# Kernel optimization log

Measured on AMD Instinct MI355X. Metric: run time of the kernel, lower is better.

The kernel has to match this reference:

```python
import jax, jax.numpy as jnp
import numpy as np

DIM = 1024
HEADS = 16
HEAD_DIM = DIM // HEADS
HIDDEN = int(DIM * 4.0)
EPS = 1e-5


def setup_inputs() -> dict:
    key = jax.random.key(0)
    ks = jax.random.split(key, 16)
    s = 0.02
    inp = {
        'x': jax.random.normal(ks[0], (2, 2048, DIM), dtype=jnp.float32),
        'g1': jnp.ones((DIM,), jnp.float32),
        'b1': jnp.zeros((DIM,), jnp.float32),
        'Wq': jax.random.normal(ks[1], (DIM, DIM)) * s,
        'bq': jnp.zeros((DIM,), jnp.float32),
        'Wk': jax.random.normal(ks[2], (DIM, DIM)) * s,
        'bk': jnp.zeros((DIM,), jnp.float32),
        'Wv': jax.random.normal(ks[3], (DIM, DIM)) * s,
        'bv': jnp.zeros((DIM,), jnp.float32),
        'Wo': jax.random.normal(ks[4], (DIM, DIM)) * s,
        'bo': jnp.zeros((DIM,), jnp.float32),
        'g2': jnp.ones((DIM,), jnp.float32),
        'b2': jnp.zeros((DIM,), jnp.float32),
        'W1': jax.random.normal(ks[5], (DIM, HIDDEN)) * s,
        'bf1': jnp.zeros((HIDDEN,), jnp.float32),
        'W2': jax.random.normal(ks[6], (HIDDEN, DIM)) * s,
        'bf2': jnp.zeros((DIM,), jnp.float32),
    }
    return inp


def _layernorm(x, g, b):
    mu = jnp.mean(x, axis=-1, keepdims=True)
    var = jnp.mean((x - mu) ** 2, axis=-1, keepdims=True)
    return (x - mu) * jax.lax.rsqrt(var + EPS) * g + b


def _block(x, g1, b1, Wq, bq, Wk, bk, Wv, bv, Wo, bo, g2, b2, W1, bf1, W2, bf2):
    B, N, C = x.shape
    h = _layernorm(x, g1, b1)
    # project and split heads: [B, H, N, D]
    q = (h @ Wq + bq).reshape(B, N, HEADS, HEAD_DIM).transpose(0, 2, 1, 3)
    k = (h @ Wk + bk).reshape(B, N, HEADS, HEAD_DIM).transpose(0, 2, 1, 3)
    v = (h @ Wv + bv).reshape(B, N, HEADS, HEAD_DIM).transpose(0, 2, 1, 3)
    scale = HEAD_DIM ** -0.5
    attn = jnp.einsum('bhqd,bhkd->bhqk', q, k) * scale
    attn = jax.nn.softmax(attn, axis=-1)
    o = jnp.einsum('bhqk,bhkd->bhqd', attn, v)
    o = o.transpose(0, 2, 1, 3).reshape(B, N, C)
    x = x + (o @ Wo + bo)
    h = _layernorm(x, g2, b2)
    h = jax.nn.gelu(h @ W1 + bf1, approximate=False)
    x = x + (h @ W2 + bf2)
    return x


def reference(x, g1, b1, Wq, bq, Wk, bk, Wv, bv, Wo, bo, g2, b2, W1, bf1, W2, bf2):
    return _block(x, g1, b1, Wq, bq, Wk, bk, Wv, bv, Wo, bo, g2, b2, W1, bf1, W2, bf2)
```

## Files before the change

### kernel.cpp

```cpp
#include <hip/hip_runtime.h>
#include <hip/hip_bf16.h>
#include <math.h>


typedef unsigned short ushort_t;
typedef short short8 __attribute__((ext_vector_type(8)));
typedef float f32x4 __attribute__((ext_vector_type(4)));

#define TOKENS 4096
#define SEQ    2048
#define DIMC   1024
#define HID    4096

__device__ __forceinline__ float bf2f(ushort_t u) {
    union { float f; unsigned int u; } c; c.u = ((unsigned int)u) << 16; return c.f;
}
__device__ __forceinline__ ushort_t f2bf(float f) {
    union { float f; unsigned int u; } c; c.f = f;
    unsigned int u = c.u;
    unsigned int r = u + 0x7fffu + ((u >> 16) & 1u);
    return (ushort_t)(r >> 16);
}
__device__ __forceinline__ float gelu_f(float x) {
    const float y = 0.79788456080286536f * (x + 0.044715f * x * x * x);
    const float t = __expf(-2.0f * fabsf(y));
    const float th = (1.0f - t) / (1.0f + t);
    return 0.5f * x * (1.0f + copysignf(th, y));
}
__device__ __forceinline__ float load_elem(const void* p, size_t i, int isbf) {
    return isbf ? bf2f(((const ushort_t*)p)[i]) : ((const float*)p)[i];
}

__global__ __launch_bounds__(256) void detect_dtype(
    const ushort_t* __restrict__ x, int* __restrict__ flag)
{
    __shared__ int bad;
    if (threadIdx.x == 0) bad = 0;
    __syncthreads();
    for (int i = threadIdx.x; i < 4096; i += 256) {
        float v = bf2f(x[i]);
        if (!(fabsf(v) <= 1e6f)) bad = 1;
    }
    __syncthreads();
    if (threadIdx.x == 0) { flag[0] = (bad == 0) ? 1 : 0; flag[1] = 1; }
}

__global__ __launch_bounds__(256) void transpose_w_all(
    const void* __restrict__ Wq, const void* __restrict__ Wk,
    const void* __restrict__ Wv, const void* __restrict__ Wo,
    const void* __restrict__ W1, const void* __restrict__ W2,
    ushort_t* __restrict__ wsq, ushort_t* __restrict__ w1t,
    ushort_t* __restrict__ w2t, const int* __restrict__ flag)
{
    __shared__ ushort_t tile[32][33];
    const int isbf = *flag;
    const int id = blockIdx.x;
    const void* in; ushort_t* out; int K, N, bx, by;
    if (id < 4096) {
        const int z = id >> 10, t = id & 1023;
        in = z == 0 ? Wq : (z == 1 ? Wk : (z == 2 ? Wv : Wo));
        out = wsq + (size_t)z * DIMC * DIMC;
        K = DIMC; N = DIMC; bx = t & 31; by = t >> 5;
    } else if (id < 8192) {
        const int t = id - 4096;
        in = W1; out = w1t; K = DIMC; N = HID;
        bx = t & 127; by = t >> 7;
    } else {
        const int t = id - 8192;
        in = W2; out = w2t; K = HID; N = DIMC;
        bx = t & 31; by = t >> 5;
    }
    const int kb = by * 32, nb = bx * 32;
    const int tx = threadIdx.x & 31, ty = threadIdx.x >> 5;
    for (int i = 0; i < 4; i++) {
        int k = kb + ty + i * 8;
        tile[ty + i * 8][tx] = f2bf(load_elem(in, (size_t)k * N + nb + tx, isbf));
    }
    __syncthreads();
    for (int i = 0; i < 4; i++) {
        int n = nb + ty + i * 8;
        out[(size_t)n * K + kb + tx] = tile[tx][ty + i * 8];
    }
}

template<int INMODE>
__global__ __launch_bounds__(256) void ln_kernel(
    const void* __restrict__ in, const void* __restrict__ g,
    const void* __restrict__ b, const int* __restrict__ flag,
    ushort_t* __restrict__ out)
{
    const int isbf = *flag;
    const int t = blockIdx.x;
    const int tid = threadIdx.x;
    const size_t base = (size_t)t * DIMC;
    float v[4];
    for (int i = 0; i < 4; i++) {
        int idx = tid + i * 256;
        v[i] = (INMODE == 1) ? ((const float*)in)[base + idx]
                             : load_elem(in, base + idx, isbf);
    }
    float s  = v[0] + v[1] + v[2] + v[3];
    float s2 = v[0]*v[0] + v[1]*v[1] + v[2]*v[2] + v[3]*v[3];
    for (int off = 1; off < 64; off <<= 1) {
        s  += __shfl_xor(s,  off);
        s2 += __shfl_xor(s2, off);
    }
    __shared__ float red[8];
    const int wave = tid >> 6, lane = tid & 63;
    if (lane == 0) { red[wave] = s; red[wave + 4] = s2; }
    __syncthreads();
    s  = red[0] + red[1] + red[2] + red[3];
    s2 = red[4] + red[5] + red[6] + red[7];
    const float mu  = s * (1.0f / DIMC);
    const float var = s2 * (1.0f / DIMC) - mu * mu;
    const float inv = rsqrtf(fmaxf(var, 0.f) + 1e-5f);
    for (int i = 0; i < 4; i++) {
        int idx = tid + i * 256;
        float o = (v[i] - mu) * inv * load_elem(g, idx, isbf) + load_elem(b, idx, isbf);
        out[base + idx] = f2bf(o);
    }
}

__global__ __launch_bounds__(256) void reduce_ln(
    const float* __restrict__ p0, const float* __restrict__ p1,
    const void* __restrict__ bias, const void* __restrict__ resid,
    float* __restrict__ x1f, const void* __restrict__ g,
    const void* __restrict__ b, const int* __restrict__ flag,
    ushort_t* __restrict__ out)
{
    const int isbf = *flag;
    const int t = blockIdx.x;
    const int tid = threadIdx.x;
    const size_t base = (size_t)t * DIMC;
    const int col = tid * 4;
    const size_t i = base + col;
    const float4 a  = *(const float4*)&p0[i];
    const float4 bb = *(const float4*)&p1[i];
    float v[4] = {a.x + bb.x, a.y + bb.y, a.z + bb.z, a.w + bb.w};
    for (int c = 0; c < 4; c++) {
        v[c] += load_elem(bias, col + c, isbf);
        v[c] += load_elem(resid, i + c, isbf);
    }
    *(float4*)&x1f[i] = make_float4(v[0], v[1], v[2], v[3]);

    float s  = v[0] + v[1] + v[2] + v[3];
    float s2 = v[0]*v[0] + v[1]*v[1] + v[2]*v[2] + v[3]*v[3];
    for (int off = 1; off < 64; off <<= 1) {
        s  += __shfl_xor(s,  off);
        s2 += __shfl_xor(s2, off);
    }
    __shared__ float red[8];
    const int wave = tid >> 6, lane = tid & 63;
    if (lane == 0) { red[wave] = s; red[wave + 4] = s2; }
    __syncthreads();
    s  = red[0] + red[1] + red[2] + red[3];
    s2 = red[4] + red[5] + red[6] + red[7];
    const float mu  = s * (1.0f / DIMC);
    const float var = s2 * (1.0f / DIMC) - mu * mu;
    const float inv = rsqrtf(fmaxf(var, 0.f) + 1e-5f);
    ushort_t ob[4];
    for (int c = 0; c < 4; c++) {
        float o = (v[c] - mu) * inv * load_elem(g, col + c, isbf)
                + load_elem(b, col + c, isbf);
        ob[c] = f2bf(o);
    }
    unsigned int lo = (unsigned int)ob[0] | ((unsigned int)ob[1] << 16);
    unsigned int hi = (unsigned int)ob[2] | ((unsigned int)ob[3] << 16);
    *(uint2*)&out[i] = make_uint2(lo, hi);
}

template<int BN, int RES, int ACT, int OUTF, int NBUF>
__global__ __launch_bounds__(256) void gemm_bt(
    const ushort_t* __restrict__ A, const ushort_t* __restrict__ BT,
    const void* __restrict__ bias0, const void* __restrict__ bias1,
    const void* __restrict__ bias2, const void* __restrict__ resid,
    void* __restrict__ out0, void* __restrict__ out1, void* __restrict__ out2,
    int M, int N, int K, int Ksub, const int* __restrict__ flag)
{
    constexpr int BM   = 128;
    constexpr int JF   = BN / 32;
    constexpr int ASEG = BM / 16;
    constexpr int SPW  = (BM + BN) / 64;
    __shared__ __align__(16) ushort_t As[NBUF][BM][32];
    __shared__ __align__(16) ushort_t Bs[NBUF][BN][32];
    const int isbf = *flag;
    const int tid = threadIdx.x, lane = tid & 63, wave = tid >> 6;

    int bx, by;
    {
        const int gx = gridDim.x, gy = gridDim.y;
        const int nwg = gx * gy;
        const int orig = blockIdx.y * gx + blockIdx.x;
        const int cpx = nwg >> 3;
        const int swz = (orig & 7) * cpx + (orig >> 3);
        bx = swz % gx;
        by = swz / gx;
    }
    const int m0 = by * BM, n0 = bx * BN;
    const int wm = (wave & 1) * 64;
    const int wn = (wave >> 1) * (BN / 2);
    const int lm = lane & 15, quad = lane >> 4;

    const void* biasp = bias0;
    void* outp = out0;
    int nout = N;
    int colmask = 0x7fffffff;
    int sel = 0;
    if (OUTF == 3) {
        sel = n0 >> 10;
        biasp = sel == 0 ? bias0 : (sel == 1 ? bias1 : bias2);
        outp  = sel == 0 ? out0  : (sel == 1 ? out1  : out2);
        nout = 1024; colmask = 1023;
    }
    int kbeg = 0;
    if (OUTF == 4) {
        kbeg = blockIdx.z * Ksub;
        outp = blockIdx.z ? out1 : out0;
    }

    f32x4 acc[4][JF];
    for (int i = 0; i < 4; i++)
        for (int j = 0; j < JF; j++)
            acc[i][j] = (f32x4){0.f, 0.f, 0.f, 0.f};

    const int lsw  = lane ^ ((lane >> 3) & 7);
    const int lrow = lsw >> 2;
    const int lcol = (lsw & 3) * 8;
    const int srd  = (4 * lm + quad);
    const int srz  = srd ^ ((srd >> 3) & 7);
    const int rsw  = srz >> 2;
    const int csw  = (srz & 3) * 8;

    const ushort_t* gpp[SPW];
    ushort_t* lpp[NBUF][SPW];
#pragma unroll
    for (int s = 0; s < SPW; s++) {
        const int seg = wave * SPW + s;
        if (seg < ASEG) {
            gpp[s] = &A[(size_t)(m0 + seg * 16 + lrow) * K + kbeg + lcol];
#pragma unroll
            for (int bfi = 0; bfi < NBUF; bfi++) lpp[bfi][s] = &As[bfi][seg * 16][0];
        } else {
            gpp[s] = &BT[(size_t)(n0 + (seg - ASEG) * 16 + lrow) * K + kbeg + lcol];
#pragma unroll
            for (int bfi = 0; bfi < NBUF; bfi++) lpp[bfi][s] = &Bs[bfi][(seg - ASEG) * 16][0];
        }
    }

#define GEMM_STAGE(BUF, T)                                                    \
    {                                                                         \
        _Pragma("unroll")                                                     \
        for (int s = 0; s < SPW; s++)                                         \
            __builtin_amdgcn_global_load_lds(                                 \
                (const __attribute__((address_space(1))) unsigned int*)       \
                    (gpp[s] + (size_t)(T) * 32),                              \
                (__attribute__((address_space(3))) unsigned int*)lpp[BUF][s], \
                16, 0, 0);                                                    \
    }

#define GEMM_COMPUTE(BUF)                                                     \
    {                                                                         \
        short8 af[4], bfr[JF];                                                \
        _Pragma("unroll")                                                     \
        for (int i = 0; i < 4; i++)                                           \
            af[i] = *(const short8*)&As[BUF][wm + i * 16 + rsw][csw];         \
        _Pragma("unroll")                                                     \
        for (int j = 0; j < JF; j++)                                          \
            bfr[j] = *(const short8*)&Bs[BUF][wn + j * 16 + rsw][csw];        \
        _Pragma("unroll")                                                     \
        for (int i = 0; i < 4; i++)                                           \
            _Pragma("unroll")                                                 \
            for (int j = 0; j < JF; j++)                                      \
                acc[i][j] = __builtin_amdgcn_mfma_f32_16x16x32_bf16(          \
                    af[i], bfr[j], acc[i][j], 0, 0, 0);                       \
    }

#define GEMM_STEP(BC, BS, T)                                                  \
    if ((T) < nt) {                                                           \
        if ((T) + 1 < nt) {                                                   \
            if constexpr (SPW == 3)                                           \
                asm volatile("s_waitcnt vmcnt(3) lgkmcnt(0)" ::: "memory");   \
            else                                                              \
                asm volatile("s_waitcnt vmcnt(4) lgkmcnt(0)" ::: "memory");   \
        } else {                                                              \
            asm volatile("s_waitcnt vmcnt(0) lgkmcnt(0)" ::: "memory");       \
        }                                                                     \
        __builtin_amdgcn_s_barrier();                                         \
        __builtin_amdgcn_sched_barrier(0);                                    \
        if ((T) + 2 < nt) GEMM_STAGE(BS, (T) + 2);                            \
        __builtin_amdgcn_s_setprio(1);                                        \
        GEMM_COMPUTE(BC);                                                     \
        __builtin_amdgcn_s_setprio(0);                                        \
    }

    const int nt = Ksub / 32;
    if constexpr (NBUF == 3) {
        GEMM_STAGE(0, 0);
        GEMM_STAGE(1, 1);
        for (int t = 0; t < nt; t += 3) {
            GEMM_STEP(0, 2, t);
            GEMM_STEP(1, 0, t + 1);
            GEMM_STEP(2, 1, t + 2);
        }
    } else {
        GEMM_STAGE(0, 0);
        __syncthreads();
        for (int t = 0; t < nt; t += 2) {
            GEMM_STAGE(1, t + 1);
            GEMM_COMPUTE(0);
            __syncthreads();
            if (t + 2 < nt) GEMM_STAGE(0, t + 2);
            GEMM_COMPUTE(1);
            __syncthreads();
        }
    }
#undef GEMM_STEP
#undef GEMM_STAGE
#undef GEMM_COMPUTE

    if (OUTF == 3 && sel == 2) {
        for (int j = 0; j < JF; j++) {
            const int colo = (n0 + wn + j * 16 + lm) & 1023;
            const float bv = load_elem(biasp, colo, isbf);
            for (int i = 0; i < 4; i++) {
                const int token = m0 + wm + i * 16 + quad * 4;
                const int bb = token >> 11, ss = token & 2047;
                unsigned int lo = (unsigned int)f2bf(acc[i][j][0] + bv)
                                | ((unsigned int)f2bf(acc[i][j][1] + bv) << 16);
                unsigned int hi = (unsigned int)f2bf(acc[i][j][2] + bv)
                                | ((unsigned int)f2bf(acc[i][j][3] + bv) << 16);
                *(uint2*)&((ushort_t*)outp)[(size_t)((bb << 10) + colo) * SEQ + ss] =
                    make_uint2(lo, hi);
            }
        }
        return;
    }

    for (int j = 0; j < JF; j++) {
        const int col  = n0 + wn + j * 16 + lm;
        const int colo = col & colmask;
        const float bv = (OUTF == 4) ? 0.f : load_elem(biasp, colo, isbf);
        for (int i = 0; i < 4; i++) {
            const int rbase = m0 + wm + i * 16 + quad * 4;
            for (int r = 0; r < 4; r++) {
                const size_t oi = (size_t)(rbase + r) * nout + colo;
                float v2 = acc[i][j][r] + bv;
                if (ACT == 1) v2 = gelu_f(v2);
                if (RES == 1) v2 += load_elem(resid, oi, isbf);
                if (RES == 2) v2 += ((const float*)resid)[oi];
                if (OUTF == 1 || OUTF == 4) { ((float*)outp)[oi] = v2; }
                else if (OUTF == 2) {
                    if (isbf) ((ushort_t*)outp)[oi] = f2bf(v2);
                    else      ((float*)outp)[oi] = v2;
                }
                else                { ((ushort_t*)outp)[oi] = f2bf(v2); }
            }
        }
    }
}

template<int RESRAW, int OUTF32>
__global__ __launch_bounds__(256) void splitk_reduce(
    const float* __restrict__ p0, const float* __restrict__ p1,
    const void* __restrict__ bias, const void* __restrict__ resid,
    void* __restrict__ out, const int* __restrict__ flag)
{
    const int isbf = *flag;
    const size_t i = ((size_t)blockIdx.x * 256 + threadIdx.x) * 4;
    const float4 a = *(const float4*)&p0[i];
    const float4 b = *(const float4*)&p1[i];
    const int col = (int)(i & 1023);
    float v[4] = {a.x + b.x, a.y + b.y, a.z + b.z, a.w + b.w};
    for (int c = 0; c < 4; c++) {
        v[c] += load_elem(bias, col + c, isbf);
        v[c] += RESRAW ? load_elem(resid, i + c, isbf) : ((const float*)resid)[i + c];
    }
    if (OUTF32) {
        *(float4*)&((float*)out)[i] = make_float4(v[0], v[1], v[2], v[3]);
    } else if (isbf) {
        unsigned int lo = (unsigned int)f2bf(v[0]) | ((unsigned int)f2bf(v[1]) << 16);
        unsigned int hi = (unsigned int)f2bf(v[2]) | ((unsigned int)f2bf(v[3]) << 16);
        *(uint2*)&((ushort_t*)out)[i] = make_uint2(lo, hi);
    } else {
        *(float4*)&((float*)out)[i] = make_float4(v[0], v[1], v[2], v[3]);
    }
}

__global__ __launch_bounds__(256) void attn_kernel(
    const ushort_t* __restrict__ q, const ushort_t* __restrict__ k,
    const ushort_t* __restrict__ vt, ushort_t* __restrict__ o)
{
    const int bh = blockIdx.x;
    const int b  = bh >> 4, h = bh & 15;
    const int q0 = blockIdx.y * 128;
    const int tid = threadIdx.x, lane = tid & 63, wave = tid >> 6;
    const int lm = lane & 15, quad = lane >> 4;

    __shared__ ushort_t Qs[128][72];
    __shared__ ushort_t Ks[64][72];
    __shared__ ushort_t Vt[64][72];
    typedef ushort_t PsRow[32][72];
    PsRow* Ps = reinterpret_cast<PsRow*>(&Qs[0][0]);

    const size_t base  = ((size_t)b * SEQ) * DIMC + h * 64;
    const size_t vbase = ((size_t)b * DIMC + h * 64) * SEQ;

    {
        const int er0 = (tid * 8) >> 6;
        const int ec0 = (tid * 8) & 63;
        for (int half = 0; half < 4; half++) {
            const int r = er0 + half * 32;
            short8 qq = *(const short8*)&q[base + (size_t)(q0 + r) * DIMC + ec0];
            short8 qs;
            for (int i = 0; i < 8; i++)
                qs[i] = (short)f2bf(bf2f((ushort_t)qq[i]) * 0.18033688011112042f);
            *(short8*)&Qs[r][ec0] = qs;
        }
    }
    __syncthreads();

    short8 qf[2][2];
    for (int qh = 0; qh < 2; qh++)
        for (int ks = 0; ks < 2; ks++)
            qf[qh][ks] = *(const short8*)&Qs[wave * 32 + qh * 16 + lm][quad * 8 + ks * 32];

    short8 onef;
    for (int i = 0; i < 8; i++) onef[i] = (short)0x3F80;

    f32x4 oacc[4][2], lacc[2];
    for (int j = 0; j < 4; j++)
        for (int qh = 0; qh < 2; qh++) oacc[j][qh] = (f32x4){0.f, 0.f, 0.f, 0.f};
    lacc[0] = (f32x4){0.f, 0.f, 0.f, 0.f};
    lacc[1] = (f32x4){0.f, 0.f, 0.f, 0.f};

    const int er = (tid * 8) >> 6;
    const int ec = (tid * 8) & 63;
    const int dd = tid >> 2;
    const int kg = tid & 3;

    short8 kreg0, kreg1, vreg0, vreg1;
    {
        kreg0 = *(const short8*)&k[base + (size_t)(er) * DIMC + ec];
        kreg1 = *(const short8*)&k[base + (size_t)(er + 32) * DIMC + ec];
        const size_t vsrc = vbase + (size_t)dd * SEQ + kg * 16;
        vreg0 = *(const short8*)&vt[vsrc];
        vreg1 = *(const short8*)&vt[vsrc + 8];
    }

    for (int kt = 0; kt < SEQ / 64; kt++) {
        __syncthreads();
        *(short8*)&Ks[er][ec]          = kreg0;
        *(short8*)&Ks[er + 32][ec]     = kreg1;
        *(short8*)&Vt[dd][kg * 16]     = vreg0;
        *(short8*)&Vt[dd][kg * 16 + 8] = vreg1;
        __syncthreads();
        if (kt + 1 < SEQ / 64) {
            const int kn = (kt + 1) * 64;
            kreg0 = *(const short8*)&k[base + (size_t)(kn + er) * DIMC + ec];
            kreg1 = *(const short8*)&k[base + (size_t)(kn + er + 32) * DIMC + ec];
            const size_t vsrc = vbase + (size_t)dd * SEQ + kn + kg * 16;
            vreg0 = *(const short8*)&vt[vsrc];
            vreg1 = *(const short8*)&vt[vsrc + 8];
        }

        f32x4 st[4][2];
        for (int j = 0; j < 4; j++)
            for (int qh = 0; qh < 2; qh++) st[j][qh] = (f32x4){0.f, 0.f, 0.f, 0.f};
        for (int ks = 0; ks < 2; ks++) {
            for (int j = 0; j < 4; j++) {
                short8 kf = *(const short8*)&Ks[j * 16 + lm][quad * 8 + ks * 32];
                for (int qh = 0; qh < 2; qh++)
                    st[j][qh] = __builtin_amdgcn_mfma_f32_16x16x32_bf16(kf, qf[qh][ks], st[j][qh], 0, 0, 0);
            }
        }

        for (int j = 0; j < 4; j++)
            for (int qh = 0; qh < 2; qh++) {
                unsigned int u0 = __float_as_uint(__builtin_amdgcn_exp2f(st[j][qh][0]));
                unsigned int u1 = __float_as_uint(__builtin_amdgcn_exp2f(st[j][qh][1]));
                unsigned int u2 = __float_as_uint(__builtin_amdgcn_exp2f(st[j][qh][2]));
                unsigned int u3 = __float_as_uint(__builtin_amdgcn_exp2f(st[j][qh][3]));
                unsigned int lo = (u1 & 0xffff0000u) | (u0 >> 16);
                unsigned int hi = (u3 & 0xffff0000u) | (u2 >> 16);
                *(uint2*)&Ps[wave][qh * 16 + lm][j * 16 + quad * 4] = make_uint2(lo, hi);
            }

        for (int ks = 0; ks < 2; ks++) {
            for (int qh = 0; qh < 2; qh++) {
                short8 pf = *(const short8*)&Ps[wave][qh * 16 + lm][quad * 8 + ks * 32];
                lacc[qh] = __builtin_amdgcn_mfma_f32_16x16x32_bf16(pf, onef, lacc[qh], 0, 0, 0);
                for (int j = 0; j < 4; j++) {
                    short8 vf = *(const short8*)&Vt[j * 16 + lm][quad * 8 + ks * 32];
                    oacc[j][qh] = __builtin_amdgcn_mfma_f32_16x16x32_bf16(pf, vf, oacc[j][qh], 0, 0, 0);
                }
            }
        }
    }

    float rinv[2][4];
    for (int qh = 0; qh < 2; qh++)
        for (int r = 0; r < 4; r++) rinv[qh][r] = 1.0f / fmaxf(lacc[qh][r], 1e-30f);

    for (int j = 0; j < 4; j++)
        for (int qh = 0; qh < 2; qh++)
            for (int r = 0; r < 4; r++) {
                const int row = q0 + wave * 32 + qh * 16 + quad * 4 + r;
                o[base + (size_t)row * DIMC + j * 16 + lm] = f2bf(oacc[j][qh][r] * rinv[qh][r]);
            }
}

extern "C" void kernel_launch(void* const* d_in, const int* in_sizes, int n_in,
                              void* d_out, int out_size, void* d_ws, size_t ws_size,
                              hipStream_t stream)
{
    const void* x   = d_in[0];
    const void* g1  = d_in[1];
    const void* b1  = d_in[2];
    const void* Wq  = d_in[3];
    const void* bq  = d_in[4];
    const void* Wk  = d_in[5];
    const void* bk  = d_in[6];
    const void* Wv  = d_in[7];
    const void* bv  = d_in[8];
    const void* Wo  = d_in[9];
    const void* bo  = d_in[10];
    const void* g2  = d_in[11];
    const void* b2  = d_in[12];
    const void* W1  = d_in[13];
    const void* bf1 = d_in[14];
    const void* W2  = d_in[15];
    const void* bf2 = d_in[16];

    const size_t SZ_TOKD_BF = (size_t)TOKENS * DIMC * 2;
    const size_t SZ_TOKD_F  = (size_t)TOKENS * DIMC * 4;
    const size_t SZ_W_SQ    = (size_t)DIMC * DIMC * 2;
    const size_t SZ_W_FF    = (size_t)DIMC * HID * 2;
    const size_t SZ_FF1     = (size_t)TOKENS * HID * 2;

    char* ws = (char*)d_ws;
    size_t off = 0;
    int*      flag = (int*)(ws + off);       off += 256;
    ushort_t* h    = (ushort_t*)(ws + off);  off += SZ_TOKD_BF;
    ushort_t* qb   = (ushort_t*)(ws + off);  off += SZ_TOKD_BF;
    ushort_t* kb_  = (ushort_t*)(ws + off);  off += SZ_TOKD_BF;
    ushort_t* ao   = (ushort_t*)(ws + off);  off += SZ_TOKD_BF;
    ushort_t* vtg  = (ushort_t*)(ws + off);  off += SZ_TOKD_BF;
    float*    x1f  = (float*)qb;
    float*    pa   = (float*)qb;
    float*    p0   = (float*)ao;
    ushort_t* wqt  = (ushort_t*)(ws + off);  off += SZ_W_SQ;
    ushort_t* wkt  = (ushort_t*)(ws + off);  off += SZ_W_SQ;
    ushort_t* wvt  = (ushort_t*)(ws + off);  off += SZ_W_SQ;
    ushort_t* wot  = (ushort_t*)(ws + off);  off += SZ_W_SQ;
    ushort_t* w1t  = (ushort_t*)(ws + off);  off += SZ_W_FF;
    ushort_t* w2t  = (ushort_t*)(ws + off);  off += SZ_W_FF;
    ushort_t* ff1  = (ushort_t*)(ws + off);  off += SZ_FF1;
    float*    p1   = (float*)(ws + off);     off += SZ_TOKD_F;
    if (ws_size < off) return;

    (void)wkt; (void)wvt;

    detect_dtype<<<1, 256, 0, stream>>>((const ushort_t*)x, flag);

    transpose_w_all<<<12288, 256, 0, stream>>>(Wq, Wk, Wv, Wo, W1, W2,
                                               wqt, w1t, w2t, flag);

    ln_kernel<0><<<TOKENS, 256, 0, stream>>>(x, g1, b1, flag, h);

    gemm_bt<128, 0, 0, 3, 3><<<dim3(24, 32), 256, 0, stream>>>(
        h, wqt, bq, bk, bv, nullptr, qb, kb_, vtg, TOKENS, 3072, DIMC, DIMC, flag);

    attn_kernel<<<dim3(32, 16), 256, 0, stream>>>(qb, kb_, vtg, ao);

    gemm_bt<64, 0, 0, 4, 3><<<dim3(16, 32, 2), 256, 0, stream>>>(
        ao, wot, nullptr, nullptr, nullptr, nullptr, pa, p1, nullptr,
        TOKENS, DIMC, DIMC, DIMC / 2, flag);

    reduce_ln<<<TOKENS, 256, 0, stream>>>(
        pa, p1, bo, x, x1f, g2, b2, flag, h);

    gemm_bt<128, 0, 1, 0, 3><<<dim3(32, 32), 256, 0, stream>>>(
        h, w1t, bf1, nullptr, nullptr, nullptr, ff1, nullptr, nullptr,
        TOKENS, HID, DIMC, DIMC, flag);

    gemm_bt<64, 0, 0, 4, 3><<<dim3(16, 32, 2), 256, 0, stream>>>(
        ff1, w2t, nullptr, nullptr, nullptr, nullptr, p0, p1, nullptr,
        TOKENS, DIMC, HID, HID / 2, flag);

    splitk_reduce<0, 0><<<TOKENS * DIMC / 1024, 256, 0, stream>>>(
        p0, p1, bf2, x1f, d_out, flag);
}
```

Measured before the change: 397.6 us.

## Halve attention query tile to 64 rows and swizzle block order

The attention kernel now handles 64 query rows per block (16 per wave) instead of 128, doubling the grid to 1024 blocks. A block-index swizzle groups adjacent blocks onto the same head to improve K/V cache reuse. The aim is more parallelism and occupancy across the CUs, at the cost of loading each K/V tile twice as often per query. The split-K GEMM also gains support for up to four z-slices, but no launch uses more than two.

Result: slower. 415.7 us (+4.6%).

```diff
diff --git a/kernel.cpp b/kernel.cpp
--- a/kernel.cpp
+++ b/kernel.cpp
@@ -214,8 +214,9 @@
     }
     int kbeg = 0;
     if (OUTF == 4) {
-        kbeg = blockIdx.z * Ksub;
-        outp = blockIdx.z ? out1 : out0;
+        const int z = blockIdx.z;
+        kbeg = z * Ksub;
+        outp = z == 0 ? out0 : (z == 1 ? out1 : (z == 2 ? out2 : (void*)resid));
     }
 
     f32x4 acc[4][JF];
@@ -390,16 +391,22 @@
     const ushort_t* __restrict__ q, const ushort_t* __restrict__ k,
     const ushort_t* __restrict__ vt, ushort_t* __restrict__ o)
 {
-    const int bh = blockIdx.x;
+    int qtile, bh;
+    {
+        const int orig = blockIdx.y * 32 + blockIdx.x;
+        const int swz = (orig & 7) * 128 + (orig >> 3);
+        qtile = swz & 31;
+        bh    = swz >> 5;
+    }
     const int b  = bh >> 4, h = bh & 15;
-    const int q0 = blockIdx.y * 128;
+    const int q0 = qtile * 64;
     const int tid = threadIdx.x, lane = tid & 63, wave = tid >> 6;
     const int lm = lane & 15, quad = lane >> 4;
 
-    __shared__ ushort_t Qs[128][72];
+    __shared__ ushort_t Qs[64][72];
     __shared__ ushort_t Ks[64][72];
     __shared__ ushort_t Vt[64][72];
-    typedef ushort_t PsRow[32][72];
+    typedef ushort_t PsRow[16][72];
     PsRow* Ps = reinterpret_cast<PsRow*>(&Qs[0][0]);
 
     const size_t base  = ((size_t)b * SEQ) * DIMC + h * 64;
@@ -408,7 +415,7 @@
     {
         const int er0 = (tid * 8) >> 6;
         const int ec0 = (tid * 8) & 63;
-        for (int half = 0; half < 4; half++) {
+        for (int half = 0; half < 2; half++) {
             const int r = er0 + half * 32;
             short8 qq = *(const short8*)&q[base + (size_t)(q0 + r) * DIMC + ec0];
             short8 qs;
@@ -419,19 +426,16 @@
     }
     __syncthreads();
 
-    short8 qf[2][2];
-    for (int qh = 0; qh < 2; qh++)
-        for (int ks = 0; ks < 2; ks++)
-            qf[qh][ks] = *(const short8*)&Qs[wave * 32 + qh * 16 + lm][quad * 8 + ks * 32];
+    short8 qf[2];
+    for (int ks = 0; ks < 2; ks++)
+        qf[ks] = *(const short8*)&Qs[wave * 16 + lm][quad * 8 + ks * 32];
 
     short8 onef;
     for (int i = 0; i < 8; i++) onef[i] = (short)0x3F80;
 
-    f32x4 oacc[4][2], lacc[2];
-    for (int j = 0; j < 4; j++)
-        for (int qh = 0; qh < 2; qh++) oacc[j][qh] = (f32x4){0.f, 0.f, 0.f, 0.f};
-    lacc[0] = (f32x4){0.f, 0.f, 0.f, 0.f};
-    lacc[1] = (f32x4){0.f, 0.f, 0.f, 0.f};
+    f32x4 oacc[4], lacc;
+    for (int j = 0; j < 4; j++) oacc[j] = (f32x4){0.f, 0.f, 0.f, 0.f};
+    lacc = (f32x4){0.f, 0.f, 0.f, 0.f};
 
     const int er = (tid * 8) >> 6;
     const int ec = (tid * 8) & 63;
@@ -463,50 +467,43 @@
             vreg1 = *(const short8*)&vt[vsrc + 8];
         }
 
-        f32x4 st[4][2];
-        for (int j = 0; j < 4; j++)
-            for (int qh = 0; qh < 2; qh++) st[j][qh] = (f32x4){0.f, 0.f, 0.f, 0.f};
+        f32x4 st[4];
+        for (int j = 0; j < 4; j++) st[j] = (f32x4){0.f, 0.f, 0.f, 0.f};
         for (int ks = 0; ks < 2; ks++) {
             for (int j = 0; j < 4; j++) {
                 short8 kf = *(const short8*)&Ks[j * 16 + lm][quad * 8 + ks * 32];
-                for (int qh = 0; qh < 2; qh++)
-                    st[j][qh] = __builtin_amdgcn_mfma_f32_16x16x32_bf16(kf, qf[qh][ks], st[j][qh], 0, 0, 0);
+                st[j] = __builtin_amdgcn_mfma_f32_16x16x32_bf16(kf, qf[ks], st[j], 0, 0, 0);
             }
         }
 
-        for (int j = 0; j < 4; j++)
-            for (int qh = 0; qh < 2; qh++) {
-                unsigned int u0 = __float_as_uint(__builtin_amdgcn_exp2f(st[j][qh][0]));
-                unsigned int u1 = __float_as_uint(__builtin_amdgcn_exp2f(st[j][qh][1]));
-                unsigned int u2 = __float_as_uint(__builtin_amdgcn_exp2f(st[j][qh][2]));
-                unsigned int u3 = __float_as_uint(__builtin_amdgcn_exp2f(st[j][qh][3]));
-                unsigned int lo = (u1 & 0xffff0000u) | (u0 >> 16);
-                unsigned int hi = (u3 & 0xffff0000u) | (u2 >> 16);
-                *(uint2*)&Ps[wave][qh * 16 + lm][j * 16 + quad * 4] = make_uint2(lo, hi);
+        for (int j = 0; j < 4; j++) {
+            unsigned int u0 = __float_as_uint(__builtin_amdgcn_exp2f(st[j][0]));
+            unsigned int u1 = __float_as_uint(__builtin_amdgcn_exp2f(st[j][1]));
+            unsigned int u2 = __float_as_uint(__builtin_amdgcn_exp2f(st[j][2]));
+            unsigned int u3 = __float_as_uint(__builtin_amdgcn_exp2f(st[j][3]));
+            unsigned int lo = (u1 & 0xffff0000u) | (u0 >> 16);
+            unsigned int hi = (u3 & 0xffff0000u) | (u2 >> 16);
+            *(uint2*)&Ps[wave][lm][j * 16 + quad * 4] = make_uint2(lo, hi);
+        }
+
+        for (int ks = 0; ks < 2; ks++) {
+            short8 pf = *(const short8*)&Ps[wave][lm][quad * 8 + ks * 32];
+            lacc = __builtin_amdgcn_mfma_f32_16x16x32_bf16(pf, onef, lacc, 0, 0, 0);
+            for (int j = 0; j < 4; j++) {
+                short8 vf = *(const short8*)&Vt[j * 16 + lm][quad * 8 + ks * 32];
+                oacc[j] = __builtin_amdgcn_mfma_f32_16x16x32_bf16(pf, vf, oacc[j], 0, 0, 0);
             }
-
-        for (int ks = 0; ks < 2; ks++) {
-            for (int qh = 0; qh < 2; qh++) {
-                short8 pf = *(const short8*)&Ps[wave][qh * 16 + lm][quad * 8 + ks * 32];
-                lacc[qh] = __builtin_amdgcn_mfma_f32_16x16x32_bf16(pf, onef, lacc[qh], 0, 0, 0);
-                for (int j = 0; j < 4; j++) {
-                    short8 vf = *(const short8*)&Vt[j * 16 + lm][quad * 8 + ks * 32];
-                    oacc[j][qh] = __builtin_amdgcn_mfma_f32_16x16x32_bf16(pf, vf, oacc[j][qh], 0, 0, 0);
-                }
-            }
-        }
-    }
-
-    float rinv[2][4];
-    for (int qh = 0; qh < 2; qh++)
-        for (int r = 0; r < 4; r++) rinv[qh][r] = 1.0f / fmaxf(lacc[qh][r], 1e-30f);
+        }
+    }
+
+    float rinv[4];
+    for (int r = 0; r < 4; r++) rinv[r] = 1.0f / fmaxf(lacc[r], 1e-30f);
 
     for (int j = 0; j < 4; j++)
-        for (int qh = 0; qh < 2; qh++)
-            for (int r = 0; r < 4; r++) {
-                const int row = q0 + wave * 32 + qh * 16 + quad * 4 + r;
-                o[base + (size_t)row * DIMC + j * 16 + lm] = f2bf(oacc[j][qh][r] * rinv[qh][r]);
-            }
+        for (int r = 0; r < 4; r++) {
+            const int row = q0 + wave * 16 + quad * 4 + r;
+            o[base + (size_t)row * DIMC + j * 16 + lm] = f2bf(oacc[j][r] * rinv[r]);
+        }
 }
 
 extern "C" void kernel_launch(void* const* d_in, const int* in_sizes, int n_in,
@@ -570,7 +567,7 @@
     gemm_bt<128, 0, 0, 3, 3><<<dim3(24, 32), 256, 0, stream>>>(
         h, wqt, bq, bk, bv, nullptr, qb, kb_, vtg, TOKENS, 3072, DIMC, DIMC, flag);
 
-    attn_kernel<<<dim3(32, 16), 256, 0, stream>>>(qb, kb_, vtg, ao);
+    attn_kernel<<<dim3(32, 32), 256, 0, stream>>>(qb, kb_, vtg, ao);
 
     gemm_bt<64, 0, 0, 4, 3><<<dim3(16, 32, 2), 256, 0, stream>>>(
         ao, wot, nullptr, nullptr, nullptr, nullptr, pa, p1, nullptr,
```

## Swizzle attention K/V shared tiles and extend split-K output selection

Applied to the files above, without the earlier changes.

Replaces the padded 72-wide K and V^T shared-memory tiles in the attention kernel with unpadded 32-wide half tiles and an XOR swizzle (the same pattern the GEMM uses), so the MFMA fragment reads avoid bank conflicts and LDS use drops. The GEMM split-K path now picks among four output buffers by blockIdx.z instead of two, allowing a deeper K split, though the host launch that would use it is not shown. The swizzle adds some index arithmetic per thread, and the write-side mapping must match the read side exactly or results will be wrong.

New measurement: 398.9 us. No clear change (+0.3%).

```diff
diff --git a/kernel.cpp b/kernel.cpp
--- a/kernel.cpp
+++ b/kernel.cpp
@@ -214,8 +214,9 @@
     }
     int kbeg = 0;
     if (OUTF == 4) {
-        kbeg = blockIdx.z * Ksub;
-        outp = blockIdx.z ? out1 : out0;
+        const int z = blockIdx.z;
+        kbeg = z * Ksub;
+        outp = z == 0 ? out0 : (z == 1 ? out1 : (z == 2 ? out2 : (void*)resid));
     }
 
     f32x4 acc[4][JF];
@@ -397,8 +398,8 @@
     const int lm = lane & 15, quad = lane >> 4;
 
     __shared__ ushort_t Qs[128][72];
-    __shared__ ushort_t Ks[64][72];
-    __shared__ ushort_t Vt[64][72];
+    __shared__ __align__(16) ushort_t Ks2[2][64][32];
+    __shared__ __align__(16) ushort_t Vt2[2][64][32];
     typedef ushort_t PsRow[32][72];
     PsRow* Ps = reinterpret_cast<PsRow*>(&Qs[0][0]);
 
@@ -435,8 +436,25 @@
 
     const int er = (tid * 8) >> 6;
     const int ec = (tid * 8) & 63;
+    const int half_k = ec >> 5;
+    const int chk_k  = (ec & 31) >> 3;
+    const int ks_s   = 4 * (er & 15) + chk_k;
+    const int ks_z   = ks_s ^ ((ks_s >> 3) & 7);
+    const int kw_r   = (er & ~15) + (ks_z >> 2);
+    const int kw_c   = (ks_z & 3) * 8;
+
     const int dd = tid >> 2;
     const int kg = tid & 3;
+    const int half_v = kg >> 1;
+    const int chv0 = 2 * (kg & 1);
+    const int vs0 = 4 * (dd & 15) + chv0,     vz0 = vs0 ^ ((vs0 >> 3) & 7);
+    const int vs1 = 4 * (dd & 15) + chv0 + 1, vz1 = vs1 ^ ((vs1 >> 3) & 7);
+    const int vw_r0 = (dd & ~15) + (vz0 >> 2), vw_c0 = (vz0 & 3) * 8;
+    const int vw_r1 = (dd & ~15) + (vz1 >> 2), vw_c1 = (vz1 & 3) * 8;
+
+    const int srd = 4 * lm + quad;
+    const int srz = srd ^ ((srd >> 3) & 7);
+    const int rsw = srz >> 2, csw = (srz & 3) * 8;
 
     short8 kreg0, kreg1, vreg0, vreg1;
     {
@@ -449,10 +467,10 @@
 
     for (int kt = 0; kt < SEQ / 64; kt++) {
         __syncthreads();
-        *(short8*)&Ks[er][ec]          = kreg0;
-        *(short8*)&Ks[er + 32][ec]     = kreg1;
-        *(short8*)&Vt[dd][kg * 16]     = vreg0;
-        *(short8*)&Vt[dd][kg * 16 + 8] = vreg1;
+        *(short8*)&Ks2[half_k][kw_r][kw_c]      = kreg0;
+        *(short8*)&Ks2[half_k][kw_r + 32][kw_c] = kreg1;
+        *(short8*)&Vt2[half_v][vw_r0][vw_c0]    = vreg0;
+        *(short8*)&Vt2[half_v][vw_r1][vw_c1]    = vreg1;
         __syncthreads();
         if (kt + 1 < SEQ / 64) {
             const int kn = (kt + 1) * 64;
@@ -468,7 +486,7 @@
             for (int qh = 0; qh < 2; qh++) st[j][qh] = (f32x4){0.f, 0.f, 0.f, 0.f};
         for (int ks = 0; ks < 2; ks++) {
             for (int j = 0; j < 4; j++) {
-                short8 kf = *(const short8*)&Ks[j * 16 + lm][quad * 8 + ks * 32];
+                short8 kf = *(const short8*)&Ks2[ks][j * 16 + rsw][csw];
                 for (int qh = 0; qh < 2; qh++)
                     st[j][qh] = __builtin_amdgcn_mfma_f32_16x16x32_bf16(kf, qf[qh][ks], st[j][qh], 0, 0, 0);
             }
@@ -490,7 +508,7 @@
                 short8 pf = *(const short8*)&Ps[wave][qh * 16 + lm][quad * 8 + ks * 32];
                 lacc[qh] = __builtin_amdgcn_mfma_f32_16x16x32_bf16(pf, onef, lacc[qh], 0, 0, 0);
                 for (int j = 0; j < 4; j++) {
-                    short8 vf = *(const short8*)&Vt[j * 16 + lm][quad * 8 + ks * 32];
+                    short8 vf = *(const short8*)&Vt2[ks][j * 16 + rsw][csw];
                     oacc[j][qh] = __builtin_amdgcn_mfma_f32_16x16x32_bf16(pf, vf, oacc[j][qh], 0, 0, 0);
                 }
             }
```
